# Performance work log

Hardware: AMD Instinct MI355X
Metric: run time of the kernel (lower is better)

The kernel has to match this reference:

```python
import jax, jax.numpy as jnp
import numpy as np

T, B, D, V, E = 512, 128, 512, 33, 128  # time, batch, hidden/enc dim, vocab, embed dim


def setup_inputs() -> dict:
    key = jax.random.key(0)
    ks = jax.random.split(key, 9)
    s = 0.05  # weight init scale, keeps activations sane
    return {
        "enc_h": jax.random.normal(ks[0], (T, B, D), dtype=jnp.float32),
        "W_emb": jax.random.normal(ks[1], (V, E), dtype=jnp.float32) * s,
        "b_emb": jax.random.normal(ks[2], (E,), dtype=jnp.float32) * s,
        "W_ih": jax.random.normal(ks[3], (E, 4 * D), dtype=jnp.float32) * s,
        "W_hh": jax.random.normal(ks[4], (D, 4 * D), dtype=jnp.float32) * s,
        "b_ih": jax.random.normal(ks[5], (4 * D,), dtype=jnp.float32) * s,
        "b_hh": jax.random.normal(ks[6], (4 * D,), dtype=jnp.float32) * s,
        "W_out": jax.random.normal(ks[7], (2 * D, V), dtype=jnp.float32) * s,
        "b_out": jax.random.normal(ks[8], (V,), dtype=jnp.float32) * s,
    }


def reference(enc_h, W_emb, b_emb, W_ih, W_hh, b_ih, b_hh, W_out, b_out):
    # self.y is a zeros buffer that is never updated, so the embed output is
    # constant across timesteps: embed(zeros) = b_emb broadcast to [B, E].
    y_emb = jnp.zeros((B, V), enc_h.dtype) @ W_emb + b_emb  # [B, E]

    def lstm_cell(x, h, c):
        g = x @ W_ih + b_ih + h @ W_hh + b_hh  # [B, 4D]
        i, f, gg, o = jnp.split(g, 4, axis=-1)  # torch LSTMCell gate order
        i, f, o = jax.nn.sigmoid(i), jax.nn.sigmoid(f), jax.nn.sigmoid(o)
        c_new = f * c + i * jnp.tanh(gg)
        h_new = o * jnp.tanh(c_new)
        return h_new, c_new

    def step(carry, hidden):  # hidden: [B, D]
        h, c, c_t = carry
        h, c = lstm_cell(y_emb, h, c)
        # Attention (faithful to the original, including raw-score denominator):
        score = hidden.T @ h                                   # [D, D]
        a_t = jnp.exp(score) / jnp.sum(score, axis=0)          # [D, D]
        # the python loop `for a in a_t: c_t += a * h_e` == sum rows, broadcast
        w = jnp.sum(a_t, axis=0)                               # [D]
        c_t = c_t + w[None, :] * hidden                        # [B, D] (stateful buffer)
        comb = jnp.concatenate([h, c_t], axis=1)               # [B, 2D]
        y_hat = jax.nn.log_softmax(comb @ W_out + b_out, axis=1)
        return (h, c, c_t), y_hat

    init = (jnp.zeros((B, D), enc_h.dtype),
            jnp.zeros((B, D), enc_h.dtype),
            jnp.zeros((B, D), enc_h.dtype))
    _, preds = jax.lax.scan(step, init, enc_h)  # [T, B, V]
    return preds
```

## Files before the change

kernel.cpp:

```cpp
#include <hip/hip_runtime.h>
#include <math.h>

constexpr int T_ = 512, B_ = 128, D_ = 512, V_ = 33, E_ = 128;
constexpr int G4 = 4 * D_;
constexpr int BD = B_ * D_;
constexpr int BV = B_ * V_;
constexpr int TWO_D = 2 * D_;
constexpr int WIMG_HALF = 1048576;

typedef __attribute__((ext_vector_type(8))) short short8;
typedef __attribute__((ext_vector_type(4))) float floatx4;

__device__ inline short f2bf(float f) {
    unsigned u = __float_as_uint(f);
    unsigned r = (u + 0x7fff + ((u >> 16) & 1)) >> 16;
    return (short)r;
}
__device__ inline float bf2f(short s) {
    return __uint_as_float(((unsigned)(unsigned short)s) << 16);
}

__global__ void prep_kernel(const float* __restrict__ b_emb, const float* __restrict__ W_ih,
                            const float* __restrict__ b_ih, const float* __restrict__ b_hh,
                            const float* __restrict__ W_out,
                            float* __restrict__ g0, float* __restrict__ WoT) {
    int idx = blockIdx.x * 256 + threadIdx.x;
    if (idx < G4) {
        float acc = b_ih[idx] + b_hh[idx];
        for (int e = 0; e < E_; ++e) acc = fmaf(b_emb[e], W_ih[e * G4 + idx], acc);
        g0[idx] = acc;
    } else {
        int k = idx - G4;
        if (k < V_ * TWO_D) {
            int v = k / TWO_D, j = k % TWO_D;
            WoT[v * TWO_D + j] = W_out[j * V_ + v];
        }
    }
}

__global__ void prep2_kernel(const float* __restrict__ Whh, short* __restrict__ Wimg) {
    int idx = blockIdx.x * 256 + threadIdx.x;
    int G = idx & 2047, k = idx >> 11;
    float v = Whh[(size_t)k * G4 + G];
    short hi = f2bf(v);
    short lo = f2bf(v - bf2f(hi));
    int g = G >> 9, cc = G & 511, n = cc >> 4, c = cc & 15;
    int kt = k >> 5, kg = (k >> 3) & 3, j = k & 7;
    int lane = kg * 16 + c;
    size_t dst = ((size_t)((n * 4 + g) * 16 + kt) * 64 + lane) * 8 + j;
    Wimg[dst] = hi;
    Wimg[dst + WIMG_HALF] = lo;
}

__global__ void rowsum_kernel(const float* __restrict__ enc, double* __restrict__ rowsum) {
    int wave = threadIdx.x >> 6, lane = threadIdx.x & 63;
    int row = blockIdx.x * 4 + wave;
    const float* p = enc + (size_t)row * D_;
    double s = 0.0;
    #pragma unroll
    for (int k = 0; k < 8; ++k) s += (double)p[k * 64 + lane];
    for (int off = 32; off; off >>= 1) s += __shfl_down(s, off, 64);
    if (lane == 0) rowsum[row] = s;
}

__global__ void __launch_bounds__(256, 1) lstm_step(const short* __restrict__ Wimg,
                                                    const float* __restrict__ g0,
                                                    float* __restrict__ Hs,
                                                    short* __restrict__ hb,
                                                    int t) {
    __shared__ short Alds[16384];
    __shared__ float xch[4][64][4];
    const int tid = threadIdx.x;
    const int l = tid & 63, g = tid >> 6;
    const int m = blockIdx.x & 7, n = blockIdx.x >> 3;
    const int col = l & 15, kg = l >> 4;
    const float g0v = g0[g * 512 + n * 16 + col];
    const short* __restrict__ bbase = Wimg + ((size_t)((n * 4 + g) * 16) * 64 + l) * 8;
    const int epos = (m * 16 + kg * 4 + g) * 512 + n * 16 + col;

    floatx4 acc = {0.f, 0.f, 0.f, 0.f};
    if (t > 0) {
        {
            const short* ah = hb + (size_t)((t - 1) & 1) * 131072 + m * 8192;
            const short* al = ah + 65536;
            #pragma unroll
            for (int it = 0; it < 4; ++it) {
                int u = it * 256 + tid;
                int s = (u & ~63) | ((u & 63) ^ ((u >> 6) & 7));
                *(short8*)&Alds[s * 8]        = *(const short8*)&ah[u * 8];
                *(short8*)&Alds[8192 + s * 8] = *(const short8*)&al[u * 8];
            }
        }
        __syncthreads();
        #pragma unroll
        for (int kt = 0; kt < 16; ++kt) {
            int sA = ((col << 6) | ((kt * 4 + kg) ^ (col & 7))) * 8;
            short8 ahi = *(const short8*)&Alds[sA];
            short8 alo = *(const short8*)&Alds[8192 + sA];
            short8 bh = *(const short8*)(bbase + kt * 512);
            short8 bl = *(const short8*)(bbase + WIMG_HALF + kt * 512);
            acc = __builtin_amdgcn_mfma_f32_16x16x32_bf16(ahi, bh, acc, 0, 0, 0);
            acc = __builtin_amdgcn_mfma_f32_16x16x32_bf16(ahi, bl, acc, 0, 0, 0);
            acc = __builtin_amdgcn_mfma_f32_16x16x32_bf16(alo, bh, acc, 0, 0, 0);
        }
    }
    xch[g][l][0] = acc[0] + g0v;
    xch[g][l][1] = acc[1] + g0v;
    xch[g][l][2] = acc[2] + g0v;
    xch[g][l][3] = acc[3] + g0v;
    __syncthreads();
    {
        float ip = xch[0][l][g];
        float fp = xch[1][l][g];
        float gp = xch[2][l][g];
        float op = xch[3][l][g];
        float* cst = (float*)(hb + 2 * 131072);
        short* hw = hb + (size_t)(t & 1) * 131072;
        float i_ = 1.f / (1.f + expf(-ip));
        float f_ = 1.f / (1.f + expf(-fp));
        float gg = tanhf(gp);
        float o_ = 1.f / (1.f + expf(-op));
        float cprev = (t > 0) ? cst[epos] : 0.f;
        float c_new = f_ * cprev + i_ * gg;
        cst[epos] = c_new;
        float h = o_ * tanhf(c_new);
        Hs[(size_t)t * BD + epos] = h;
        short hi = f2bf(h);
        short lo = f2bf(h - bf2f(hi));
        hw[epos] = hi;
        hw[65536 + epos] = lo;
    }
}

__global__ void score_kernel(const float* __restrict__ enc, const float* __restrict__ Hs,
                             const double* __restrict__ rowsum, float* __restrict__ wout) {
    __shared__ float Hj[B_][68];
    __shared__ float Ei[B_][36];
    __shared__ float numer[64];
    const int tid = threadIdx.x;
    const int t  = blockIdx.x >> 3;
    const int j0 = (blockIdx.x & 7) * 64;
    for (int i = 0; i < 32; ++i) {
        int idx = i * 256 + tid;
        int bb = idx >> 6, jl = idx & 63;
        Hj[bb][jl] = Hs[(size_t)t * BD + bb * D_ + j0 + jl];
    }
    if (tid < 64) numer[tid] = 0.f;
    __syncthreads();
    const int ti = tid & 15;
    const int tj = tid >> 4;
    for (int itile = 0; itile < 16; ++itile) {
        int i0 = itile * 32;
        for (int i = 0; i < 16; ++i) {
            int idx = i * 256 + tid;
            int bb = idx >> 5, il = idx & 31;
            Ei[bb][il] = enc[(size_t)t * BD + bb * D_ + i0 + il];
        }
        __syncthreads();
        float a00=0,a01=0,a02=0,a03=0,a10=0,a11=0,a12=0,a13=0;
        #pragma unroll 4
        for (int bb = 0; bb < B_; ++bb) {
            float2 e2 = *(const float2*)&Ei[bb][ti * 2];
            float4 h4 = *(const float4*)&Hj[bb][tj * 4];
            a00 = fmaf(e2.x, h4.x, a00); a01 = fmaf(e2.x, h4.y, a01);
            a02 = fmaf(e2.x, h4.z, a02); a03 = fmaf(e2.x, h4.w, a03);
            a10 = fmaf(e2.y, h4.x, a10); a11 = fmaf(e2.y, h4.y, a11);
            a12 = fmaf(e2.y, h4.z, a12); a13 = fmaf(e2.y, h4.w, a13);
        }
        float v0 = expf(a00) + expf(a10);
        float v1 = expf(a01) + expf(a11);
        float v2 = expf(a02) + expf(a12);
        float v3 = expf(a03) + expf(a13);
        #pragma unroll
        for (int off = 1; off < 16; off <<= 1) {
            v0 += __shfl_xor(v0, off, 16);
            v1 += __shfl_xor(v1, off, 16);
            v2 += __shfl_xor(v2, off, 16);
            v3 += __shfl_xor(v3, off, 16);
        }
        if (ti == 0) {
            numer[tj * 4 + 0] += v0;
            numer[tj * 4 + 1] += v1;
            numer[tj * 4 + 2] += v2;
            numer[tj * 4 + 3] += v3;
        }
        __syncthreads();
    }
    if (tid < 64) {
        const double* rs = rowsum + t * B_;
        double dd = 0.0;
        for (int bb = 0; bb < B_; ++bb) dd += rs[bb] * (double)Hj[bb][tid];
        wout[t * D_ + j0 + tid] = (float)((double)numer[tid] / dd);
    }
}

__global__ void ufuse_kernel(const float* __restrict__ enc, const float* __restrict__ Hs,
                             const float* __restrict__ wbuf, const float* __restrict__ WoT,
                             float* __restrict__ u, float* __restrict__ hlog) {
    int wave = threadIdx.x >> 6, lane = threadIdx.x & 63;
    int row = blockIdx.x * 4 + wave;
    int t = row >> 7, b = row & 127;
    const float* Erow = enc + (size_t)row * D_;
    const float* Hrow = Hs  + (size_t)row * D_;
    const float* wrow = wbuf + t * D_;
    float ar[8], hr[8];
    #pragma unroll
    for (int k = 0; k < 8; ++k) {
        int j = k * 64 + lane;
        ar[k] = wrow[j] * Erow[j];
        hr[k] = Hrow[j];
    }
    for (int v = 0; v < V_; ++v) {
        const float* wo = WoT + v * TWO_D;
        float su = 0.f, sh = 0.f;
        #pragma unroll
        for (int k = 0; k < 8; ++k) {
            int j = k * 64 + lane;
            su = fmaf(ar[k], wo[D_ + j], su);
            sh = fmaf(hr[k], wo[j], sh);
        }
        for (int off = 32; off; off >>= 1) {
            su += __shfl_down(su, off, 64);
            sh += __shfl_down(sh, off, 64);
        }
        if (lane == 0) {
            u[(size_t)t * BV + b * V_ + v] = su;
            hlog[(size_t)row * V_ + v] = sh;
        }
    }
}

__global__ void cumsum_kernel(float* __restrict__ u) {
    int bv = blockIdx.x * 256 + threadIdx.x;
    if (bv >= BV) return;
    float acc = 0.f;
    for (int t = 0; t < T_; ++t) {
        acc += u[(size_t)t * BV + bv];
        u[(size_t)t * BV + bv] = acc;
    }
}

__global__ void final_kernel(const float* __restrict__ hlog, const float* __restrict__ u,
                             const float* __restrict__ b_out, float* __restrict__ out) {
    int row = blockIdx.x * 256 + threadIdx.x;
    float logit[V_];
    float m = -INFINITY;
    #pragma unroll
    for (int v = 0; v < V_; ++v) {
        float x = hlog[(size_t)row * V_ + v] + u[(size_t)row * V_ + v] + b_out[v];
        logit[v] = x;
        m = fmaxf(m, x);
    }
    float s = 0.f;
    #pragma unroll
    for (int v = 0; v < V_; ++v) s += expf(logit[v] - m);
    float lse = m + logf(s);
    #pragma unroll
    for (int v = 0; v < V_; ++v) out[(size_t)row * V_ + v] = logit[v] - lse;
}

extern "C" void kernel_launch(void* const* d_in, const int* in_sizes, int n_in,
                              void* d_out, int out_size, void* d_ws, size_t ws_size,
                              hipStream_t stream) {
    const float* enc   = (const float*)d_in[0];
    const float* b_emb = (const float*)d_in[2];
    const float* W_ih  = (const float*)d_in[3];
    const float* W_hh  = (const float*)d_in[4];
    const float* b_ih  = (const float*)d_in[5];
    const float* b_hh  = (const float*)d_in[6];
    const float* W_out = (const float*)d_in[7];
    const float* b_out = (const float*)d_in[8];
    float* out = (float*)d_out;

    char* p = (char*)d_ws;
    double* rowsum = (double*)p;              p += sizeof(double) * (size_t)T_ * B_;
    float* Hs      = (float*)p;               p += sizeof(float) * (size_t)T_ * BD;
    float* wbuf    = (float*)p;               p += sizeof(float) * (size_t)T_ * D_;
    float* u       = (float*)p;               p += sizeof(float) * (size_t)T_ * BV;
    float* hlog    = (float*)p;               p += sizeof(float) * (size_t)T_ * BV;
    float* g0      = (float*)p;               p += sizeof(float) * G4;
    float* WoT     = (float*)p;               p += sizeof(float) * V_ * TWO_D;
    short* Wimg    = (short*)p;               p += sizeof(short) * 2 * WIMG_HALF;
    short* hb      = (short*)p;               p += sizeof(short) * (2 * 131072 + 2 * BD);

    prep_kernel<<<(G4 + V_ * TWO_D + 255) / 256, 256, 0, stream>>>(b_emb, W_ih, b_ih, b_hh, W_out, g0, WoT);
    prep2_kernel<<<(G4 * D_) / 256, 256, 0, stream>>>(W_hh, Wimg);
    rowsum_kernel<<<T_ * B_ / 4, 256, 0, stream>>>(enc, rowsum);
    for (int t = 0; t < T_; ++t) {
        lstm_step<<<256, 256, 0, stream>>>(Wimg, g0, Hs, hb, t);
    }
    score_kernel<<<T_ * 8, 256, 0, stream>>>(enc, Hs, rowsum, wbuf);
    ufuse_kernel<<<T_ * B_ / 4, 256, 0, stream>>>(enc, Hs, wbuf, WoT, u, hlog);
    cumsum_kernel<<<(BV + 255) / 256, 256, 0, stream>>>(u);
    final_kernel<<<T_ * B_ / 256, 256, 0, stream>>>(hlog, u, b_out, out);
}
```

Before: 4.357 ms.

## Replace per-timestep LSTM launches with persistent cooperative kernel and flag barriers

The 512 separate lstm_step launches become one cooperative persistent kernel that loops over time. Blocks in the same row group m sync through per-step atomic counter flags in global memory, and the cell state now lives in a register instead of global memory. At startup the kernel checks which XCC each block landed on, and skips the thread fences when every m group sits on a single XCC. This removes launch overhead and global barriers per step, at the cost of spin-waiting and reliance on co-residency and cache-coherence assumptions.

```diff
diff --git a/kernel.cpp b/kernel.cpp
--- a/kernel.cpp
+++ b/kernel.cpp
@@ -1,4 +1,5 @@
 #include <hip/hip_runtime.h>
+#include <hip/hip_cooperative_groups.h>
 #include <math.h>
 
 constexpr int T_ = 512, B_ = 128, D_ = 512, V_ = 33, E_ = 128;
@@ -63,13 +64,15 @@
     if (lane == 0) rowsum[row] = s;
 }
 
-__global__ void __launch_bounds__(256, 1) lstm_step(const short* __restrict__ Wimg,
-                                                    const float* __restrict__ g0,
-                                                    float* __restrict__ Hs,
-                                                    short* __restrict__ hb,
-                                                    int t) {
+__global__ void __launch_bounds__(256, 1) lstm_persist(const short* __restrict__ Wimg,
+                                                       const float* __restrict__ g0,
+                                                       float* __restrict__ Hs,
+                                                       short* __restrict__ hb,
+                                                       unsigned* __restrict__ bar,
+                                                       unsigned* __restrict__ xinfo) {
     __shared__ short Alds[16384];
     __shared__ float xch[4][64][4];
+    __shared__ int fastflag;
     const int tid = threadIdx.x;
     const int l = tid & 63, g = tid >> 6;
     const int m = blockIdx.x & 7, n = blockIdx.x >> 3;
@@ -78,57 +81,102 @@
     const short* __restrict__ bbase = Wimg + ((size_t)((n * 4 + g) * 16) * 64 + l) * 8;
     const int epos = (m * 16 + kg * 4 + g) * 512 + n * 16 + col;
 
-    floatx4 acc = {0.f, 0.f, 0.f, 0.f};
-    if (t > 0) {
+    if (tid == 0) {
+        unsigned xcc = __builtin_amdgcn_s_getreg(6164) & 0xFu;
+        __hip_atomic_fetch_or(&xinfo[m * 16], 1u << xcc, __ATOMIC_RELAXED, __HIP_MEMORY_SCOPE_AGENT);
+        __hip_atomic_fetch_add(&xinfo[128], 1u, __ATOMIC_RELAXED, __HIP_MEMORY_SCOPE_AGENT);
+        while (__hip_atomic_load(&xinfo[128], __ATOMIC_RELAXED, __HIP_MEMORY_SCOPE_AGENT) < 256u)
+            __builtin_amdgcn_s_sleep(1);
+        unsigned orall = 0;
+        int ok = 1;
+        for (int i = 0; i < 8; ++i) {
+            unsigned mk = __hip_atomic_load(&xinfo[i * 16], __ATOMIC_RELAXED, __HIP_MEMORY_SCOPE_AGENT);
+            orall |= mk;
+            if (__popc(mk) != 1) ok = 0;
+        }
+        if (orall != 0xFFu) ok = 0;
+        fastflag = ok;
+    }
+    __syncthreads();
+    const bool fast = (fastflag != 0);
+
+    float creg = 0.f;
+
+    for (int t = 0; t < T_; ++t) {
+        floatx4 acc = {0.f, 0.f, 0.f, 0.f};
+        if (t > 0) {
+            if (l == 0) {
+                const unsigned* flag = bar + (size_t)((t - 1) * 8 + m) * 16;
+                while (__hip_atomic_load(flag, __ATOMIC_RELAXED, __HIP_MEMORY_SCOPE_AGENT) < 32u)
+                    __builtin_amdgcn_s_sleep(2);
+                if (!fast) __threadfence();
+            }
+            __syncthreads();
+            {
+                const short* ah = hb + (size_t)((t - 1) & 1) * 131072 + m * 8192;
+                const short* al = ah + 65536;
+                #pragma unroll
+                for (int it = 0; it < 4; ++it) {
+                    int u = it * 256 + tid;
+                    int s = (u & ~63) | ((u & 63) ^ ((u >> 6) & 7));
+                    const unsigned long long* ahq = (const unsigned long long*)(ah + u * 8);
+                    const unsigned long long* alq = (const unsigned long long*)(al + u * 8);
+                    unsigned long long h0 = *(const volatile unsigned long long*)(ahq + 0);
+                    unsigned long long h1 = *(const volatile unsigned long long*)(ahq + 1);
+                    unsigned long long l0 = *(const volatile unsigned long long*)(alq + 0);
+                    unsigned long long l1 = *(const volatile unsigned long long*)(alq + 1);
+                    unsigned long long* dh = (unsigned long long*)&Alds[s * 8];
+                    unsigned long long* dl = (unsigned long long*)&Alds[8192 + s * 8];
+                    dh[0] = h0; dh[1] = h1;
+                    dl[0] = l0; dl[1] = l1;
+                }
+            }
+            __syncthreads();
+            #pragma unroll
+            for (int kt = 0; kt < 16; ++kt) {
+                int sA = ((col << 6) | ((kt * 4 + kg) ^ (col & 7))) * 8;
+                short8 ahi = *(const short8*)&Alds[sA];
+                short8 alo = *(const short8*)&Alds[8192 + sA];
+                short8 bh = *(const short8*)(bbase + kt * 512);
+                short8 bl = *(const short8*)(bbase + WIMG_HALF + kt * 512);
+                acc = __builtin_amdgcn_mfma_f32_16x16x32_bf16(ahi, bh, acc, 0, 0, 0);
+                acc = __builtin_amdgcn_mfma_f32_16x16x32_bf16(ahi, bl, acc, 0, 0, 0);
+                acc = __builtin_amdgcn_mfma_f32_16x16x32_bf16(alo, bh, acc, 0, 0, 0);
+            }
+        }
+        xch[g][l][0] = acc[0] + g0v;
+        xch[g][l][1] = acc[1] + g0v;
+        xch[g][l][2] = acc[2] + g0v;
+        xch[g][l][3] = acc[3] + g0v;
+        __syncthreads();
         {
-            const short* ah = hb + (size_t)((t - 1) & 1) * 131072 + m * 8192;
-            const short* al = ah + 65536;
-            #pragma unroll
-            for (int it = 0; it < 4; ++it) {
-                int u = it * 256 + tid;
-                int s = (u & ~63) | ((u & 63) ^ ((u >> 6) & 7));
-                *(short8*)&Alds[s * 8]        = *(const short8*)&ah[u * 8];
-                *(short8*)&Alds[8192 + s * 8] = *(const short8*)&al[u * 8];
+            float ip = xch[0][l][g];
+            float fp = xch[1][l][g];
+            float gp = xch[2][l][g];
+            float op = xch[3][l][g];
+            short* hw = hb + (size_t)(t & 1) * 131072;
+            float i_ = 1.f / (1.f + expf(-ip));
+            float f_ = 1.f / (1.f + expf(-fp));
+            float gg = tanhf(gp);
+            float o_ = 1.f / (1.f + expf(-op));
+            float c_new = f_ * creg + i_ * gg;
+            creg = c_new;
+            float h = o_ * tanhf(c_new);
+            Hs[(size_t)t * BD + epos] = h;
+            short hi = f2bf(h);
+            short lo = f2bf(h - bf2f(hi));
+            hw[epos] = hi;
+            hw[65536 + epos] = lo;
+        }
+        if (t + 1 < T_) {
+            asm volatile("s_waitcnt vmcnt(0)" ::: "memory");
+            __syncthreads();
+            if (tid == 0) {
+                if (!fast) __threadfence();
+                __hip_atomic_fetch_add(bar + (size_t)(t * 8 + m) * 16, 1u,
+                                       __ATOMIC_RELAXED, __HIP_MEMORY_SCOPE_AGENT);
             }
         }
-        __syncthreads();
-        #pragma unroll
-        for (int kt = 0; kt < 16; ++kt) {
-            int sA = ((col << 6) | ((kt * 4 + kg) ^ (col & 7))) * 8;
-            short8 ahi = *(const short8*)&Alds[sA];
-            short8 alo = *(const short8*)&Alds[8192 + sA];
-            short8 bh = *(const short8*)(bbase + kt * 512);
-            short8 bl = *(const short8*)(bbase + WIMG_HALF + kt * 512);
-            acc = __builtin_amdgcn_mfma_f32_16x16x32_bf16(ahi, bh, acc, 0, 0, 0);
-            acc = __builtin_amdgcn_mfma_f32_16x16x32_bf16(ahi, bl, acc, 0, 0, 0);
-            acc = __builtin_amdgcn_mfma_f32_16x16x32_bf16(alo, bh, acc, 0, 0, 0);
-        }
-    }
-    xch[g][l][0] = acc[0] + g0v;
-    xch[g][l][1] = acc[1] + g0v;
-    xch[g][l][2] = acc[2] + g0v;
-    xch[g][l][3] = acc[3] + g0v;
-    __syncthreads();
-    {
-        float ip = xch[0][l][g];
-        float fp = xch[1][l][g];
-        float gp = xch[2][l][g];
-        float op = xch[3][l][g];
-        float* cst = (float*)(hb + 2 * 131072);
-        short* hw = hb + (size_t)(t & 1) * 131072;
-        float i_ = 1.f / (1.f + expf(-ip));
-        float f_ = 1.f / (1.f + expf(-fp));
-        float gg = tanhf(gp);
-        float o_ = 1.f / (1.f + expf(-op));
-        float cprev = (t > 0) ? cst[epos] : 0.f;
-        float c_new = f_ * cprev + i_ * gg;
-        cst[epos] = c_new;
-        float h = o_ * tanhf(c_new);
-        Hs[(size_t)t * BD + epos] = h;
-        short hi = f2bf(h);
-        short lo = f2bf(h - bf2f(hi));
-        hw[epos] = hi;
-        hw[65536 + epos] = lo;
     }
 }
 
@@ -282,12 +330,24 @@
     float* WoT     = (float*)p;               p += sizeof(float) * V_ * TWO_D;
     short* Wimg    = (short*)p;               p += sizeof(short) * 2 * WIMG_HALF;
     short* hb      = (short*)p;               p += sizeof(short) * (2 * 131072 + 2 * BD);
-
+    unsigned* bar  = (unsigned*)p;            p += sizeof(unsigned) * T_ * 8 * 16;
+    unsigned* xinfo = (unsigned*)p;           p += sizeof(unsigned) * 256;
+
+    hipMemsetAsync(bar, 0, sizeof(unsigned) * T_ * 8 * 16, stream);
+    hipMemsetAsync(xinfo, 0, sizeof(unsigned) * 256, stream);
     prep_kernel<<<(G4 + V_ * TWO_D + 255) / 256, 256, 0, stream>>>(b_emb, W_ih, b_ih, b_hh, W_out, g0, WoT);
     prep2_kernel<<<(G4 * D_) / 256, 256, 0, stream>>>(W_hh, Wimg);
     rowsum_kernel<<<T_ * B_ / 4, 256, 0, stream>>>(enc, rowsum);
-    for (int t = 0; t < T_; ++t) {
-        lstm_step<<<256, 256, 0, stream>>>(Wimg, g0, Hs, hb, t);
+    {
+        const short* Wimg_p = Wimg;
+        const float* g0_p   = g0;
+        float* Hs_p = Hs;
+        short* hb_p = hb;
+        unsigned* bar_p = bar;
+        unsigned* xinfo_p = xinfo;
+        void* args[] = { (void*)&Wimg_p, (void*)&g0_p, (void*)&Hs_p, (void*)&hb_p,
+                         (void*)&bar_p, (void*)&xinfo_p };
+        hipLaunchCooperativeKernel(lstm_persist, dim3(256), dim3(256), args, 0, stream);
     }
     score_kernel<<<T_ * 8, 256, 0, stream>>>(enc, Hs, rowsum, wbuf);
     ufuse_kernel<<<T_ * B_ / 4, 256, 0, stream>>>(enc, Hs, wbuf, WoT, u, hlog);
```

After: 6.928 ms. +59.0%, slower.
